# Performance work log

Hardware: AMD Instinct MI355X
Metric: run time of the kernel (lower is better)

## Reference

```python
import jax, jax.numpy as jnp
import numpy as np

D_MODEL = 2048
N_HEADS = 16
HEAD_DIM = D_MODEL // N_HEADS
ROPE_THETA = 10000.0
B, S = 2, 2048
MAX_POS = 8192


def _rope(x, position_ids):
    # x: [b, h, s, hd]; position_ids: [b, s] int
    half = HEAD_DIM // 2
    inv_freq = 1.0 / (ROPE_THETA ** (jnp.arange(0, HEAD_DIM, 2, dtype=jnp.float32) / HEAD_DIM))  # [half]
    ang = position_ids[..., None].astype(jnp.float32) * inv_freq  # [b, s, half]
    cos = jnp.concatenate([jnp.cos(ang), jnp.cos(ang)], axis=-1)[:, None]  # [b, 1, s, hd]
    sin = jnp.concatenate([jnp.sin(ang), jnp.sin(ang)], axis=-1)[:, None]
    x1, x2 = x[..., :half], x[..., half:]
    rot = jnp.concatenate([-x2, x1], axis=-1)  # rotate_half
    return x * cos + rot * sin


def setup_inputs() -> dict:
    key = jax.random.key(0)
    ks = jax.random.split(key, 6)
    wscale = 1.0 / np.sqrt(D_MODEL)
    x_sparse = jax.random.normal(ks[0], (B, S, D_MODEL), dtype=jnp.float32)
    Wq = jax.random.normal(ks[1], (D_MODEL, D_MODEL), dtype=jnp.float32) * wscale
    Wk = jax.random.normal(ks[2], (D_MODEL, D_MODEL), dtype=jnp.float32) * wscale
    Wv = jax.random.normal(ks[3], (D_MODEL, D_MODEL), dtype=jnp.float32) * wscale
    Wo = jax.random.normal(ks[4], (D_MODEL, D_MODEL), dtype=jnp.float32) * wscale
    position_ids = jnp.sort(jax.random.randint(ks[5], (B, S), 0, MAX_POS), axis=-1).astype(jnp.int64)
    return {"x_sparse": x_sparse, "Wq": Wq, "Wk": Wk, "Wv": Wv, "Wo": Wo, "position_ids": position_ids}


def reference(x_sparse, Wq, Wk, Wv, Wo, position_ids):
    b, s, d = x_sparse.shape

    def heads(W):
        return (x_sparse @ W).reshape(b, s, N_HEADS, HEAD_DIM).transpose(0, 2, 1, 3)  # [b,h,s,hd]

    q = _rope(heads(Wq), position_ids)
    k = _rope(heads(Wk), position_ids)
    v = heads(Wv)

    scores = jnp.einsum('bhqd,bhkd->bhqk', q, k) / np.float32(np.sqrt(HEAD_DIM))
    # dynamic position-based causal mask: pos_i >= pos_j, broadcast over heads
    mask = position_ids[:, None, :, None] >= position_ids[:, None, None, :]  # [b,1,s,s]
    scores = jnp.where(mask, scores, jnp.float32(-1e30))
    attn = jax.nn.softmax(scores, axis=-1)
    out = jnp.einsum('bhqk,bhkd->bhqd', attn, v)  # [b,h,s,hd]
    out = out.transpose(0, 2, 1, 3).reshape(b, s, d)
    return out @ Wo
```

## Files before the change

kernel.cpp:

```cpp
#include <hip/hip_runtime.h>
#include <stdint.h>


typedef unsigned short u16;
typedef unsigned int u32;
typedef __attribute__((ext_vector_type(8))) short bf16x8;
typedef __attribute__((ext_vector_type(4))) float f32x4;

#define SEQ 2048
#define DM 2048
#define NH 16
#define HD 128
#define SM_SCALE 0.08838834764831845f

__device__ __forceinline__ u16 f2bf(float f) {
  union { float f; uint32_t u; } v; v.f = f;
  uint32_t u = v.u + 0x7fffu + ((v.u >> 16) & 1u);
  return (u16)(u >> 16);
}
__device__ __forceinline__ float bf2f(u16 h) {
  union { uint32_t u; float f; } v; v.u = ((uint32_t)h) << 16; return v.f;
}
__device__ __forceinline__ u32 pack2(float a, float b) {
  return (u32)f2bf(a) | ((u32)f2bf(b) << 16);
}

__device__ __forceinline__ void gl2lds16(const void* g, void* l) {
  __builtin_amdgcn_global_load_lds(
      (const __attribute__((address_space(1))) uint32_t*)g,
      (__attribute__((address_space(3))) uint32_t*)l, 16, 0, 0);
}

__global__ __launch_bounds__(256) void cvt_x(const float* __restrict__ x, u16* __restrict__ xb) {
  int i = blockIdx.x * 256 + threadIdx.x;
  float4 v = ((const float4*)x)[i];
  uint2 r;
  r.x = pack2(v.x, v.y);
  r.y = pack2(v.z, v.w);
  ((uint2*)xb)[i] = r;
}

__global__ __launch_bounds__(256) void wtrans(const float* __restrict__ w0, const float* __restrict__ w1,
                                              const float* __restrict__ w2, const float* __restrict__ w3,
                                              u16* __restrict__ dst) {
  const float* W = blockIdx.z == 0 ? w0 : blockIdx.z == 1 ? w1 : blockIdx.z == 2 ? w2 : w3;
  u16* D = dst + (size_t)blockIdx.z * DM * DM;
  int k0 = blockIdx.x * 32, n0 = blockIdx.y * 32;
  __shared__ u16 t[32][33];
  int tx = threadIdx.x, ty = threadIdx.y;
#pragma unroll
  for (int i = 0; i < 32; i += 8)
    t[ty + i][tx] = f2bf(W[(size_t)(k0 + ty + i) * DM + n0 + tx]);
  __syncthreads();
#pragma unroll
  for (int i = 0; i < 32; i += 8)
    D[(size_t)(n0 + ty + i) * DM + k0 + tx] = t[tx][ty + i];
}

__device__ __forceinline__ void gemm_core(const u16* __restrict__ A, const u16* __restrict__ Bt,
                                          int m0, int n0, u16* As, u16* Bs, f32x4 acc[4][4]) {
  int tid = threadIdx.x, lane = tid & 63;
  int l15 = lane & 15, quad = lane >> 4;
  int wave = tid >> 6;
  int wm = (wave >> 1) * 64, wn = (wave & 1) * 64;
  for (int k0 = 0; k0 < DM; k0 += 64) {
#pragma unroll
    for (int i = 0; i < 4; ++i) {
      int s = i * 256 + tid;
      int row = s >> 3, c = (s & 7) ^ (row & 7);
      gl2lds16(&A[(size_t)(m0 + row) * DM + k0 + c * 8], &As[(s & ~63) * 8]);
      gl2lds16(&Bt[(size_t)(n0 + row) * DM + k0 + c * 8], &Bs[(s & ~63) * 8]);
    }
    __syncthreads();
#pragma unroll
    for (int kk = 0; kk < 2; ++kk) {
      bf16x8 af[4], bfr[4];
#pragma unroll
      for (int mt = 0; mt < 4; ++mt) {
        int row = wm + mt * 16 + l15;
        int c = (kk * 4 + quad) ^ (row & 7);
        af[mt] = *(const bf16x8*)&As[row * 64 + c * 8];
      }
#pragma unroll
      for (int nt = 0; nt < 4; ++nt) {
        int row = wn + nt * 16 + l15;
        int c = (kk * 4 + quad) ^ (row & 7);
        bfr[nt] = *(const bf16x8*)&Bs[row * 64 + c * 8];
      }
#pragma unroll
      for (int mt = 0; mt < 4; ++mt)
#pragma unroll
        for (int nt = 0; nt < 4; ++nt)
          acc[mt][nt] = __builtin_amdgcn_mfma_f32_16x16x32_bf16(af[mt], bfr[nt], acc[mt][nt], 0, 0, 0);
    }
    __syncthreads();
  }
}

__global__ __launch_bounds__(256) void qkv_gemm(const u16* __restrict__ X, const u16* __restrict__ Wt,
                                                u16* __restrict__ Qo, u16* __restrict__ Ko,
                                                u16* __restrict__ Vto) {
  __shared__ u16 As[128 * 64];
  __shared__ u16 Bs[128 * 64];
  const u16* Bt = Wt + (size_t)blockIdx.z * DM * DM;
  int n0 = blockIdx.x * 128, m0 = blockIdx.y * 128;
  f32x4 acc[4][4] = {};
  gemm_core(X, Bt, m0, n0, As, Bs, acc);
  int lane = threadIdx.x & 63, wave = threadIdx.x >> 6;
  int l15 = lane & 15, quad = lane >> 4;
  int wm = (wave >> 1) * 64, wn = (wave & 1) * 64;
  if (blockIdx.z == 2) {
    int h = n0 >> 7;
#pragma unroll
    for (int mt = 0; mt < 4; ++mt)
#pragma unroll
      for (int nt = 0; nt < 4; ++nt) {
        int tok = m0 + wm + mt * 16 + quad * 4;
        int d = wn + nt * 16 + l15;
        int b = tok >> 11, sx = tok & (SEQ - 1);
        u16* dp = &Vto[((size_t)(b * NH + h) * HD + d) * SEQ + sx];
        *(u32*)&dp[0] = pack2(acc[mt][nt][0], acc[mt][nt][1]);
        *(u32*)&dp[2] = pack2(acc[mt][nt][2], acc[mt][nt][3]);
      }
  } else {
    u16* C = blockIdx.z == 0 ? Qo : Ko;
#pragma unroll
    for (int mt = 0; mt < 4; ++mt)
#pragma unroll
      for (int nt = 0; nt < 4; ++nt)
#pragma unroll
        for (int r = 0; r < 4; ++r)
          C[(size_t)(m0 + wm + mt * 16 + quad * 4 + r) * DM + n0 + wn + nt * 16 + l15]
              = f2bf(acc[mt][nt][r]);
  }
}

__global__ __launch_bounds__(256) void proj_gemm(const u16* __restrict__ A, const u16* __restrict__ Wt,
                                                 float* __restrict__ C) {
  __shared__ u16 As[128 * 64];
  __shared__ u16 Bs[128 * 64];
  int n0 = blockIdx.x * 128, m0 = blockIdx.y * 128;
  f32x4 acc[4][4] = {};
  gemm_core(A, Wt, m0, n0, As, Bs, acc);
  int lane = threadIdx.x & 63, wave = threadIdx.x >> 6;
  int l15 = lane & 15, quad = lane >> 4;
  int wm = (wave >> 1) * 64, wn = (wave & 1) * 64;
#pragma unroll
  for (int mt = 0; mt < 4; ++mt)
#pragma unroll
    for (int nt = 0; nt < 4; ++nt)
#pragma unroll
      for (int r = 0; r < 4; ++r)
        C[(size_t)(m0 + wm + mt * 16 + quad * 4 + r) * DM + n0 + wn + nt * 16 + l15] = acc[mt][nt][r];
}

__global__ __launch_bounds__(256) void rope_k(u16* __restrict__ Q, u16* __restrict__ K,
                                              const int* __restrict__ pos) {
  uint32_t idx = blockIdx.x * 256 + threadIdx.x;
  int i = idx & 63;
  int h = (idx >> 6) & 15;
  int s = (idx >> 10) & 2047;
  int b = idx >> 21;
  u16* P = (blockIdx.y == 0) ? Q : K;
  int p = pos[b * SEQ + s];
  float inv = exp2f((float)i * -0.20762051f);
  float ang = (float)p * inv;
  float sn, cs;
  sincosf(ang, &sn, &cs);
  size_t base = ((size_t)(b * SEQ + s)) * DM + h * HD;
  float x1 = bf2f(P[base + i]), x2 = bf2f(P[base + 64 + i]);
  P[base + i] = f2bf(x1 * cs - x2 * sn);
  P[base + 64 + i] = f2bf(x2 * cs + x1 * sn);
}

__global__ __launch_bounds__(256) void attn_k(const u16* __restrict__ Q, const u16* __restrict__ K,
                                              const u16* __restrict__ Vt, const int* __restrict__ pos,
                                              u16* __restrict__ AO) {
  __shared__ u16 Ks[2][64 * 128];
  __shared__ u16 Vs[2][128 * 64];
  __shared__ int pk[2][64];
  int bx = blockIdx.x, bh = blockIdx.y;
  int b = bh >> 4, h = bh & 15;
  int qt = b ? (15 - bx) : bx;
  int tid = threadIdx.x, lane = tid & 63, wave = tid >> 6;
  int l15 = lane & 15, quad = lane >> 4;
  const int* posb = pos + b * SEQ;
  int qbase = qt * 128 + wave * 16;
  const u16* Kbase = &K[(size_t)(b * SEQ) * DM + h * HD];
  const u16* Vbase = &Vt[(size_t)(b * NH + h) * HD * SEQ];

  bf16x8 qf[2][4];
  int pq[2];
#pragma unroll
  for (int qi = 0; qi < 2; ++qi) {
#pragma unroll
    for (int kk = 0; kk < 4; ++kk)
      qf[qi][kk] = *(const bf16x8*)&Q[(size_t)(b * SEQ + qbase + qi * 64 + l15) * DM
                                      + h * HD + kk * 32 + quad * 8];
    pq[qi] = posb[qbase + qi * 64 + l15];
  }
  int pqmax = posb[qt * 128 + 127];

  int ntile = 1;
  while (ntile < 32 && posb[ntile * 64] <= pqmax) ++ntile;

#pragma unroll
  for (int i = 0; i < 4; ++i) {
    int s = i * 256 + tid;
    { int row = s >> 4, c = (s & 15) ^ (row & 15);
      gl2lds16(&Kbase[(size_t)row * DM + c * 8], &Ks[0][(s & ~63) * 8]); }
    { int row = s >> 3, c = (s & 7) ^ (row & 7);
      gl2lds16(&Vbase[(size_t)row * SEQ + c * 8], &Vs[0][(s & ~63) * 8]); }
  }
  if (tid < 64) pk[0][tid] = posb[tid];

  float m_i[2] = {-1.0e30f, -1.0e30f}, l_i[2] = {0.0f, 0.0f};
  f32x4 oacc[2][8] = {};

  for (int j = 0; j < ntile; ++j) {
    int cur = j & 1;
    __syncthreads();

    if (j + 1 < ntile) {
      int j0n = (j + 1) * 64, alt = cur ^ 1;
#pragma unroll
      for (int i = 0; i < 4; ++i) {
        int s = i * 256 + tid;
        { int row = s >> 4, c = (s & 15) ^ (row & 15);
          gl2lds16(&Kbase[(size_t)(j0n + row) * DM + c * 8], &Ks[alt][(s & ~63) * 8]); }
        { int row = s >> 3, c = (s & 7) ^ (row & 7);
          gl2lds16(&Vbase[(size_t)row * SEQ + j0n + c * 8], &Vs[alt][(s & ~63) * 8]); }
      }
      if (tid < 64) pk[alt][tid] = posb[j0n + tid];
    }

    f32x4 sacc[2][4] = {};
#pragma unroll
    for (int kk = 0; kk < 4; ++kk) {
      bf16x8 kf[4];
#pragma unroll
      for (int kt = 0; kt < 4; ++kt) {
        int row = kt * 16 + l15;
        int c = (kk * 4 + quad) ^ (row & 15);
        kf[kt] = *(const bf16x8*)&Ks[cur][row * 128 + c * 8];
      }
#pragma unroll
      for (int qi = 0; qi < 2; ++qi)
#pragma unroll
        for (int kt = 0; kt < 4; ++kt)
          sacc[qi][kt] = __builtin_amdgcn_mfma_f32_16x16x32_bf16(kf[kt], qf[qi][kk], sacc[qi][kt], 0, 0, 0);
    }

    int4 pkv[4];
#pragma unroll
    for (int kt = 0; kt < 4; ++kt) pkv[kt] = *(const int4*)&pk[cur][kt * 16 + quad * 4];

    u32 pb[2][4][2];
    float al[2];
#pragma unroll
    for (int qi = 0; qi < 2; ++qi) {
      float mx = -3.0e38f;
#pragma unroll
      for (int kt = 0; kt < 4; ++kt) {
        const int* pr = (const int*)&pkv[kt];
#pragma unroll
        for (int r = 0; r < 4; ++r) {
          float s = sacc[qi][kt][r] * SM_SCALE;
          s = (pq[qi] >= pr[r]) ? s : -1.0e30f;
          sacc[qi][kt][r] = s;
          mx = fmaxf(mx, s);
        }
      }
      mx = fmaxf(mx, __shfl_xor(mx, 16));
      mx = fmaxf(mx, __shfl_xor(mx, 32));
      float mn = fmaxf(m_i[qi], mx);
      al[qi] = __expf(m_i[qi] - mn);
      m_i[qi] = mn;
      float rs = 0.0f;
#pragma unroll
      for (int kt = 0; kt < 4; ++kt) {
        float p0 = __expf(sacc[qi][kt][0] - mn), p1 = __expf(sacc[qi][kt][1] - mn);
        float p2 = __expf(sacc[qi][kt][2] - mn), p3 = __expf(sacc[qi][kt][3] - mn);
        rs += (p0 + p1) + (p2 + p3);
        pb[qi][kt][0] = pack2(p0, p1);
        pb[qi][kt][1] = pack2(p2, p3);
      }
      rs += __shfl_xor(rs, 16);
      rs += __shfl_xor(rs, 32);
      l_i[qi] = l_i[qi] * al[qi] + rs;
#pragma unroll
      for (int dt = 0; dt < 8; ++dt) oacc[qi][dt] *= al[qi];
    }

    int base0 = l15 + ((quad & 1) << 5);
    bool hi = (quad >> 1) != 0;
#pragma unroll
    for (int kk = 0; kk < 2; ++kk) {
      bf16x8 vf[8];
#pragma unroll
      for (int dt = 0; dt < 8; ++dt) {
        int row = dt * 16 + l15;
        int c = (kk * 4 + quad) ^ (row & 7);
        vf[dt] = *(const bf16x8*)&Vs[cur][row * 64 + c * 8];
      }
#pragma unroll
      for (int qi = 0; qi < 2; ++qi) {
        u32 w[4];
#pragma unroll
        for (int wd = 0; wd < 4; ++wd) {
          int src = base0 + ((wd >> 1) << 4);
          u32 va = __shfl(pb[qi][kk * 2 + 0][wd & 1], src);
          u32 vb = __shfl(pb[qi][kk * 2 + 1][wd & 1], src);
          w[wd] = hi ? vb : va;
        }
        union { bf16x8 v; u32 u[4]; } pt;
        pt.u[0] = w[0]; pt.u[1] = w[1]; pt.u[2] = w[2]; pt.u[3] = w[3];
#pragma unroll
        for (int dt = 0; dt < 8; ++dt)
          oacc[qi][dt] = __builtin_amdgcn_mfma_f32_16x16x32_bf16(vf[dt], pt.v, oacc[qi][dt], 0, 0, 0);
      }
    }
  }

#pragma unroll
  for (int qi = 0; qi < 2; ++qi) {
    float inv = 1.0f / l_i[qi];
    u16* aop = &AO[(size_t)(b * SEQ + qbase + qi * 64 + l15) * DM + h * HD];
#pragma unroll
    for (int dt = 0; dt < 8; ++dt) {
      int col = dt * 16 + quad * 4;
      *(u32*)&aop[col]     = pack2(oacc[qi][dt][0] * inv, oacc[qi][dt][1] * inv);
      *(u32*)&aop[col + 2] = pack2(oacc[qi][dt][2] * inv, oacc[qi][dt][3] * inv);
    }
  }
}

extern "C" void kernel_launch(void* const* d_in, const int* in_sizes, int n_in,
                              void* d_out, int out_size, void* d_ws, size_t ws_size,
                              hipStream_t stream) {
  const float* x  = (const float*)d_in[0];
  const float* Wq = (const float*)d_in[1];
  const float* Wk = (const float*)d_in[2];
  const float* Wv = (const float*)d_in[3];
  const float* Wo = (const float*)d_in[4];
  const int*  pos = (const int*)d_in[5];
  float* out = (float*)d_out;

  u16* ws  = (u16*)d_ws;
  u16* xb  = ws;
  u16* wt  = xb  + (size_t)4096 * 2048;
  u16* qb  = wt  + (size_t)4 * 2048 * 2048;
  u16* kb  = qb  + (size_t)4096 * 2048;
  u16* vtb = kb  + (size_t)4096 * 2048;
  u16* aob = vtb + (size_t)4096 * 2048;

  cvt_x<<<8192, 256, 0, stream>>>(x, xb);
  wtrans<<<dim3(64, 64, 4), dim3(32, 8), 0, stream>>>(Wq, Wk, Wv, Wo, wt);
  qkv_gemm<<<dim3(16, 32, 3), 256, 0, stream>>>(xb, wt, qb, kb, vtb);
  rope_k<<<dim3(16384, 2), 256, 0, stream>>>(qb, kb, pos);
  attn_k<<<dim3(16, 32), 256, 0, stream>>>(qb, kb, vtb, pos, aob);
  proj_gemm<<<dim3(16, 32), 256, 0, stream>>>(aob, wt + (size_t)3 * 2048 * 2048, out);
}
```

Before: 469.5 us.

## Replace per-key position mask with binary-search counts and lazy softmax rescale

Each query's causal limit is computed once by binary search over the sorted positions, so masking becomes an index compare that runs only on boundary tiles instead of loading key positions into LDS every tile. The softmax now folds the scale into exp2, packs probabilities to bf16 by truncation, and skips the rescale of the accumulator when no row max grew. The double-buffer loop is unrolled into two static LDS buffers. The mask now relies on positions being sorted, and truncating to bf16 adds rounding bias.

```diff
diff --git a/kernel.cpp b/kernel.cpp
--- a/kernel.cpp
+++ b/kernel.cpp
@@ -12,6 +12,7 @@
 #define NH 16
 #define HD 128
 #define SM_SCALE 0.08838834764831845f
+#define K2LOG 0.12751743f
 
 __device__ __forceinline__ u16 f2bf(float f) {
   union { float f; uint32_t u; } v; v.f = f;
@@ -23,6 +24,10 @@
 }
 __device__ __forceinline__ u32 pack2(float a, float b) {
   return (u32)f2bf(a) | ((u32)f2bf(b) << 16);
+}
+__device__ __forceinline__ u32 pack2_trunc(float a, float b) {
+  union { float f; u32 u; } x, y; x.f = a; y.f = b;
+  return (x.u >> 16) | (y.u & 0xFFFF0000u);
 }
 
 __device__ __forceinline__ void gl2lds16(const void* g, void* l) {
@@ -176,9 +181,8 @@
 __global__ __launch_bounds__(256) void attn_k(const u16* __restrict__ Q, const u16* __restrict__ K,
                                               const u16* __restrict__ Vt, const int* __restrict__ pos,
                                               u16* __restrict__ AO) {
-  __shared__ u16 Ks[2][64 * 128];
-  __shared__ u16 Vs[2][128 * 64];
-  __shared__ int pk[2][64];
+  __shared__ u16 Ks0[64 * 128], Ks1[64 * 128];
+  __shared__ u16 Vs0[128 * 64], Vs1[128 * 64];
   int bx = blockIdx.x, bh = blockIdx.y;
   int b = bh >> 4, h = bh & 15;
   int qt = b ? (15 - bx) : bx;
@@ -189,51 +193,48 @@
   const u16* Kbase = &K[(size_t)(b * SEQ) * DM + h * HD];
   const u16* Vbase = &Vt[(size_t)(b * NH + h) * HD * SEQ];
 
+  auto prefetch = [&](int t, u16* KsD, u16* VsD) {
+#pragma unroll
+    for (int i = 0; i < 4; ++i) {
+      int s = i * 256 + tid;
+      int rk = s >> 4, ck = (s & 15) ^ (rk & 15);
+      gl2lds16(&Kbase[(size_t)(t * 64 + rk) * DM + ck * 8], &KsD[(s & ~63) * 8]);
+      int rv = s >> 3, cv = (s & 7) ^ (rv & 7);
+      gl2lds16(&Vbase[(size_t)rv * SEQ + t * 64 + cv * 8], &VsD[(s & ~63) * 8]);
+    }
+  };
+  prefetch(0, Ks0, Vs0);
+
   bf16x8 qf[2][4];
-  int pq[2];
-#pragma unroll
-  for (int qi = 0; qi < 2; ++qi) {
+#pragma unroll
+  for (int qi = 0; qi < 2; ++qi)
 #pragma unroll
     for (int kk = 0; kk < 4; ++kk)
       qf[qi][kk] = *(const bf16x8*)&Q[(size_t)(b * SEQ + qbase + qi * 64 + l15) * DM
                                       + h * HD + kk * 32 + quad * 8];
-    pq[qi] = posb[qbase + qi * 64 + l15];
-  }
-  int pqmax = posb[qt * 128 + 127];
-
-  int ntile = 1;
-  while (ntile < 32 && posb[ntile * 64] <= pqmax) ++ntile;
-
-#pragma unroll
-  for (int i = 0; i < 4; ++i) {
-    int s = i * 256 + tid;
-    { int row = s >> 4, c = (s & 15) ^ (row & 15);
-      gl2lds16(&Kbase[(size_t)row * DM + c * 8], &Ks[0][(s & ~63) * 8]); }
-    { int row = s >> 3, c = (s & 7) ^ (row & 7);
-      gl2lds16(&Vbase[(size_t)row * SEQ + c * 8], &Vs[0][(s & ~63) * 8]); }
-  }
-  if (tid < 64) pk[0][tid] = posb[tid];
+
+  auto ub = [&](int v) {
+    int c = 0;
+#pragma unroll
+    for (int st = 1024; st; st >>= 1)
+      if (posb[c + st - 1] <= v) c += st;
+    if (c == 2047 && posb[2047] <= v) c = 2048;
+    return c;
+  };
+  int cnt[2];
+  cnt[0] = ub(posb[qbase + l15]);
+  cnt[1] = ub(posb[qbase + 64 + l15]);
+  int cnt_min = ub(posb[qt * 128]);
+  int cnt_max = ub(posb[qt * 128 + 127]);
+  int ntile = (cnt_max + 63) >> 6;
 
   float m_i[2] = {-1.0e30f, -1.0e30f}, l_i[2] = {0.0f, 0.0f};
   f32x4 oacc[2][8] = {};
 
-  for (int j = 0; j < ntile; ++j) {
-    int cur = j & 1;
-    __syncthreads();
-
-    if (j + 1 < ntile) {
-      int j0n = (j + 1) * 64, alt = cur ^ 1;
-#pragma unroll
-      for (int i = 0; i < 4; ++i) {
-        int s = i * 256 + tid;
-        { int row = s >> 4, c = (s & 15) ^ (row & 15);
-          gl2lds16(&Kbase[(size_t)(j0n + row) * DM + c * 8], &Ks[alt][(s & ~63) * 8]); }
-        { int row = s >> 3, c = (s & 7) ^ (row & 7);
-          gl2lds16(&Vbase[(size_t)row * SEQ + j0n + c * 8], &Vs[alt][(s & ~63) * 8]); }
-      }
-      if (tid < 64) pk[alt][tid] = posb[j0n + tid];
-    }
-
+  int base0 = l15 + ((quad & 1) << 5);
+  bool hi_sel = (quad >> 1) != 0;
+
+  auto compute = [&](int j0, const u16* KsS, const u16* VsS) {
     f32x4 sacc[2][4] = {};
 #pragma unroll
     for (int kk = 0; kk < 4; ++kk) {
@@ -242,7 +243,7 @@
       for (int kt = 0; kt < 4; ++kt) {
         int row = kt * 16 + l15;
         int c = (kk * 4 + quad) ^ (row & 15);
-        kf[kt] = *(const bf16x8*)&Ks[cur][row * 128 + c * 8];
+        kf[kt] = *(const bf16x8*)&KsS[row * 128 + c * 8];
       }
 #pragma unroll
       for (int qi = 0; qi < 2; ++qi)
@@ -251,49 +252,52 @@
           sacc[qi][kt] = __builtin_amdgcn_mfma_f32_16x16x32_bf16(kf[kt], qf[qi][kk], sacc[qi][kt], 0, 0, 0);
     }
 
-    int4 pkv[4];
-#pragma unroll
-    for (int kt = 0; kt < 4; ++kt) pkv[kt] = *(const int4*)&pk[cur][kt * 16 + quad * 4];
-
+    bool need_mask = (j0 + 64 > cnt_min);
     u32 pb[2][4][2];
-    float al[2];
 #pragma unroll
     for (int qi = 0; qi < 2; ++qi) {
-      float mx = -3.0e38f;
-#pragma unroll
-      for (int kt = 0; kt < 4; ++kt) {
-        const int* pr = (const int*)&pkv[kt];
-#pragma unroll
-        for (int r = 0; r < 4; ++r) {
-          float s = sacc[qi][kt][r] * SM_SCALE;
-          s = (pq[qi] >= pr[r]) ? s : -1.0e30f;
-          sacc[qi][kt][r] = s;
-          mx = fmaxf(mx, s);
-        }
+      if (need_mask) {
+        int rel = cnt[qi] - j0;
+#pragma unroll
+        for (int kt = 0; kt < 4; ++kt)
+#pragma unroll
+          for (int r = 0; r < 4; ++r)
+            if (kt * 16 + quad * 4 + r >= rel) sacc[qi][kt][r] = -1.0e30f;
+      }
+      float mx = fmaxf(fmaxf(sacc[qi][0][0], sacc[qi][0][1]), fmaxf(sacc[qi][0][2], sacc[qi][0][3]));
+#pragma unroll
+      for (int kt = 1; kt < 4; ++kt) {
+        mx = fmaxf(mx, fmaxf(fmaxf(sacc[qi][kt][0], sacc[qi][kt][1]),
+                             fmaxf(sacc[qi][kt][2], sacc[qi][kt][3])));
       }
       mx = fmaxf(mx, __shfl_xor(mx, 16));
       mx = fmaxf(mx, __shfl_xor(mx, 32));
-      float mn = fmaxf(m_i[qi], mx);
-      al[qi] = __expf(m_i[qi] - mn);
-      m_i[qi] = mn;
+      float mold = m_i[qi];
+      float mn = fmaxf(mold, mx);
+      if (__any(mn > mold)) {
+        float al = exp2f((mold - mn) * K2LOG);
+        l_i[qi] *= al;
+#pragma unroll
+        for (int dt = 0; dt < 8; ++dt) oacc[qi][dt] *= al;
+        m_i[qi] = mn;
+      }
+      float nc = -m_i[qi] * K2LOG;
       float rs = 0.0f;
 #pragma unroll
       for (int kt = 0; kt < 4; ++kt) {
-        float p0 = __expf(sacc[qi][kt][0] - mn), p1 = __expf(sacc[qi][kt][1] - mn);
-        float p2 = __expf(sacc[qi][kt][2] - mn), p3 = __expf(sacc[qi][kt][3] - mn);
+        float p0 = exp2f(fmaf(sacc[qi][kt][0], K2LOG, nc));
+        float p1 = exp2f(fmaf(sacc[qi][kt][1], K2LOG, nc));
+        float p2 = exp2f(fmaf(sacc[qi][kt][2], K2LOG, nc));
+        float p3 = exp2f(fmaf(sacc[qi][kt][3], K2LOG, nc));
         rs += (p0 + p1) + (p2 + p3);
-        pb[qi][kt][0] = pack2(p0, p1);
-        pb[qi][kt][1] = pack2(p2, p3);
+        pb[qi][kt][0] = pack2_trunc(p0, p1);
+        pb[qi][kt][1] = pack2_trunc(p2, p3);
       }
       rs += __shfl_xor(rs, 16);
       rs += __shfl_xor(rs, 32);
-      l_i[qi] = l_i[qi] * al[qi] + rs;
-#pragma unroll
-      for (int dt = 0; dt < 8; ++dt) oacc[qi][dt] *= al[qi];
-    }
-
-    int base0 = l15 + ((quad & 1) << 5);
-    bool hi = (quad >> 1) != 0;
+      l_i[qi] += rs;
+    }
+
 #pragma unroll
     for (int kk = 0; kk < 2; ++kk) {
       bf16x8 vf[8];
@@ -301,7 +305,7 @@
       for (int dt = 0; dt < 8; ++dt) {
         int row = dt * 16 + l15;
         int c = (kk * 4 + quad) ^ (row & 7);
-        vf[dt] = *(const bf16x8*)&Vs[cur][row * 64 + c * 8];
+        vf[dt] = *(const bf16x8*)&VsS[row * 64 + c * 8];
       }
 #pragma unroll
       for (int qi = 0; qi < 2; ++qi) {
@@ -311,7 +315,7 @@
           int src = base0 + ((wd >> 1) << 4);
           u32 va = __shfl(pb[qi][kk * 2 + 0][wd & 1], src);
           u32 vb = __shfl(pb[qi][kk * 2 + 1][wd & 1], src);
-          w[wd] = hi ? vb : va;
+          w[wd] = hi_sel ? vb : va;
         }
         union { bf16x8 v; u32 u[4]; } pt;
         pt.u[0] = w[0]; pt.u[1] = w[1]; pt.u[2] = w[2]; pt.u[3] = w[3];
@@ -320,6 +324,16 @@
           oacc[qi][dt] = __builtin_amdgcn_mfma_f32_16x16x32_bf16(vf[dt], pt.v, oacc[qi][dt], 0, 0, 0);
       }
     }
+  };
+
+  for (int j = 0; j < ntile; j += 2) {
+    __syncthreads();
+    if (j + 1 < ntile) prefetch(j + 1, Ks1, Vs1);
+    compute(j * 64, Ks0, Vs0);
+    if (j + 1 >= ntile) break;
+    __syncthreads();
+    if (j + 2 < ntile) prefetch(j + 2, Ks0, Vs0);
+    compute((j + 1) * 64, Ks1, Vs1);
   }
 
 #pragma unroll
```

Measured after the change: 459.3 us. 2.2% less time.
